# Optimization experiments

Measured on AMD Instinct MI355X. Metric: run time of the kernel, lower is better.

The kernel has to match this reference:

```python
import jax, jax.numpy as jnp
import numpy as np

B, T, E, H, V = 128, 64, 512, 1024, 10000


def setup_inputs() -> dict:
    key = jax.random.key(0)
    ks = jax.random.split(key, 9)
    s = 0.05
    return {
        "features": jax.random.normal(ks[0], (B, E), dtype=jnp.float32),
        "captions": jax.random.randint(ks[1], (B, T), 0, V, dtype=jnp.int64),
        "embed_W": jax.random.normal(ks[2], (V, E), dtype=jnp.float32) * s,
        "W_ih": jax.random.normal(ks[3], (4 * H, E), dtype=jnp.float32) * s,
        "W_hh": jax.random.normal(ks[4], (4 * H, H), dtype=jnp.float32) * s,
        "b_ih": jax.random.normal(ks[5], (4 * H,), dtype=jnp.float32) * s,
        "b_hh": jax.random.normal(ks[6], (4 * H,), dtype=jnp.float32) * s,
        "fc_W": jax.random.normal(ks[7], (V, H), dtype=jnp.float32) * s,
        "fc_b": jax.random.normal(ks[8], (V,), dtype=jnp.float32) * s,
    }


def reference(features, captions, embed_W, W_ih, W_hh, b_ih, b_hh, fc_W, fc_b):
    # Embed captions: [B, T, E]
    cap_emb = embed_W[captions]
    # Input sequence per the original loop: t=0 -> features, t>=1 -> cap_emb[:, t]
    xs = jnp.concatenate([features[:, None, :], cap_emb[:, 1:, :]], axis=1)  # [B, T, E]
    hdim = W_hh.shape[1]
    # Precompute input contribution to gates for all steps: [T, B, 4H]
    x_gates = jnp.einsum("bte,ge->tbg", xs, W_ih) + b_ih + b_hh

    def step(carry, xg):
        h, c = carry
        g = xg + h @ W_hh.T  # [B, 4H]
        i, f, gg, o = jnp.split(g, 4, axis=-1)
        i = jax.nn.sigmoid(i)
        f = jax.nn.sigmoid(f)
        gg = jnp.tanh(gg)
        o = jax.nn.sigmoid(o)
        c = f * c + i * gg
        h = o * jnp.tanh(c)
        return (h, c), h

    bsz = features.shape[0]
    h0 = jnp.zeros((bsz, hdim), dtype=features.dtype)
    c0 = jnp.zeros((bsz, hdim), dtype=features.dtype)
    _, hs = jax.lax.scan(step, (h0, c0), x_gates)  # hs: [T, B, H]
    # Output projection per step: [B, T, V]
    out = jnp.einsum("tbh,vh->btv", hs, fc_W) + fc_b
    return out
```

## Files before the change

### kernel.cpp

```cpp
#include <hip/hip_runtime.h>
#include <math.h>

static constexpr int Bb = 128;
static constexpr int Tt = 64;
static constexpr int Ee = 512;
static constexpr int Hh = 1024;
static constexpr int Vv = 10000;
static constexpr int G  = 4 * Hh;
static constexpr int Vpad = 10112;

typedef __attribute__((ext_vector_type(8))) short short8;
typedef __attribute__((ext_vector_type(4))) float floatx4;

__device__ __forceinline__ unsigned short f2bf(float f) {
    unsigned u = __float_as_uint(f);
    return (unsigned short)((u + 0x7fffu + ((u >> 16) & 1u)) >> 16);
}

__device__ __forceinline__ void gload16(const void* g, void* l) {
    __builtin_amdgcn_global_load_lds(
        (const __attribute__((address_space(1))) void*)g,
        (__attribute__((address_space(3))) void*)l, 16, 0, 0);
}

__device__ __forceinline__ float sigmoid_fast(float x) {
    return __builtin_amdgcn_rcpf(1.f + __expf(-x));
}
__device__ __forceinline__ float tanh_fast(float x) {
    float e = __expf(-2.f * fabsf(x));
    float t = (1.f - e) * __builtin_amdgcn_rcpf(1.f + e);
    return copysignf(t, x);
}

__global__ __launch_bounds__(256)
void cvt_bf16(const float* __restrict__ s, unsigned short* __restrict__ d,
              int n, int npad) {
    int i8 = (blockIdx.x * 256 + threadIdx.x) * 8;
    if (i8 >= npad) return;
    short8 v;
    #pragma unroll
    for (int j = 0; j < 8; ++j) {
        int e = i8 + j;
        float f = (e < n) ? s[e] : 0.f;
        v[j] = (short)f2bf(f);
    }
    *reinterpret_cast<short8*>(d + i8) = v;
}

__global__ __launch_bounds__(256)
void gather_xs(const float* __restrict__ features,
               const int* __restrict__ captions,
               const float* __restrict__ embed_W,
               unsigned short* __restrict__ xs) {
    int idx = blockIdx.x * 256 + threadIdx.x;
    int m  = idx >> 6;
    int c8 = (idx & 63) * 8;
    int t = m >> 7;
    int b = m & 127;
    const float* src;
    if (t == 0) {
        src = features + (size_t)b * Ee + c8;
    } else {
        int tok = captions[(size_t)b * Tt + t];
        src = embed_W + (size_t)tok * Ee + c8;
    }
    short8 v;
    #pragma unroll
    for (int j = 0; j < 8; ++j) v[j] = (short)f2bf(src[j]);
    *reinterpret_cast<short8*>(xs + (size_t)m * Ee + c8) = v;
}

template<int BM, int BN, int MODE>
__global__ __launch_bounds__(256)
void mfma_gemm(const unsigned short* __restrict__ A,
               const unsigned short* __restrict__ Bm,
               int M, int N, int K,
               const float* __restrict__ bias0, const float* __restrict__ bias1,
               float* __restrict__ C) {
    constexpr int BK = 32;
    constexpr int FM = BM / 32;
    constexpr int FN = BN / 32;
    __shared__ unsigned short As[BM * BK];
    __shared__ unsigned short Bs[BN * BK];

    const int nwg = gridDim.x * gridDim.y;
    const int flat = blockIdx.y * gridDim.x + blockIdx.x;
    const int tix = (flat & 7) * (nwg >> 3) + (flat >> 3);
    const int bx = tix % gridDim.x;
    const int by = tix / gridDim.x;

    const int tid  = threadIdx.x;
    const int wid  = tid >> 6;
    const int lane = tid & 63;
    const int wr = wid >> 1, wc = wid & 1;
    const int row0 = bx * BM;
    const int col0 = by * BN;
    const int l15 = lane & 15;
    const int kq  = lane >> 4;

    floatx4 acc[FM][FN];
    #pragma unroll
    for (int i = 0; i < FM; ++i)
        #pragma unroll
        for (int j = 0; j < FN; ++j) acc[i][j] = (floatx4)0.f;

    constexpr int LA = (BM * BK) / (256 * 8);
    constexpr int LB = (BN * BK) / (256 * 8);

    for (int k0 = 0; k0 < K; k0 += BK) {
        #pragma unroll
        for (int i = 0; i < LA; ++i) {
            int e = i * 2048 + tid * 8;
            int r = e >> 5, k = e & 31;
            gload16(A + (size_t)(row0 + r) * K + k0 + k, &As[e]);
        }
        #pragma unroll
        for (int i = 0; i < LB; ++i) {
            int e = i * 2048 + tid * 8;
            int r = e >> 5, k = e & 31;
            gload16(Bm + (size_t)(col0 + r) * K + k0 + k, &Bs[e]);
        }
        __syncthreads();

        short8 af[FM], bfr[FN];
        #pragma unroll
        for (int i = 0; i < FM; ++i) {
            int r = wr * (BM / 2) + i * 16 + l15;
            af[i] = *reinterpret_cast<const short8*>(&As[r * BK + kq * 8]);
        }
        #pragma unroll
        for (int j = 0; j < FN; ++j) {
            int c = wc * (BN / 2) + j * 16 + l15;
            bfr[j] = *reinterpret_cast<const short8*>(&Bs[c * BK + kq * 8]);
        }
        #pragma unroll
        for (int i = 0; i < FM; ++i)
            #pragma unroll
            for (int j = 0; j < FN; ++j)
                acc[i][j] = __builtin_amdgcn_mfma_f32_16x16x32_bf16(
                    af[i], bfr[j], acc[i][j], 0, 0, 0);
        __syncthreads();
    }

    #pragma unroll
    for (int i = 0; i < FM; ++i) {
        #pragma unroll
        for (int j = 0; j < FN; ++j) {
            #pragma unroll
            for (int q = 0; q < 4; ++q) {
                int m = row0 + wr * (BM / 2) + i * 16 + kq * 4 + q;
                int n = col0 + wc * (BN / 2) + j * 16 + l15;
                float v = acc[i][j][q];
                if (MODE == 0) {
                    C[(size_t)m * N + n] = v + bias0[n] + bias1[n];
                } else {
                    if (n < N) {
                        int t = m >> 7, b = m & 127;
                        C[(size_t)b * (Tt * Vv) + (size_t)t * Vv + n] = v + bias0[n];
                    }
                }
            }
        }
    }
}

__global__ __launch_bounds__(256)
void lstm_persist(const unsigned short* __restrict__ whhb,
                  const float* __restrict__ xg,
                  unsigned short* __restrict__ hsb,
                  unsigned* __restrict__ flags) {
    __shared__ unsigned short Wlds[64 * Hh];
    __shared__ float redsum[8 * 3 * 4 * 64];
    const int tid  = threadIdx.x;
    const int w    = blockIdx.x;
    const int wg_m = w & 3;
    const int wg_n = w >> 2;
    const int wave = tid >> 6;
    const int lane = tid & 63;
    const int l15  = lane & 15;
    const int kq   = lane >> 4;

    for (int i = 0; i < 32; ++i) {
        int e8 = i * 256 + tid;
        int q = e8 >> 6, gc = e8 & 63;
        int grow = (gc >> 4) * Hh + wg_n * 16 + (gc & 15);
        short8 v = *reinterpret_cast<const short8*>(
            whhb + (size_t)grow * Hh + q * 8);
        *reinterpret_cast<short8*>(&Wlds[(q * 64 + gc) * 8]) = v;
    }
    __syncthreads();

    const int row0 = wg_m * 32;
    const int hcol = wg_n * 16 + l15;
    const int lrA = (wave >> 1) * 16 + kq * 4 + ((wave & 1) * 2);
    const int lrB = lrA + 1;
    unsigned* myctr = flags + (size_t)(wg_m * 8 + (wg_n >> 3)) * 16;
    float cell0 = 0.f, cell1 = 0.f;

    float xa[2][4], xb[2][4];
    {
        const float* xrA = xg + (size_t)(row0 + lrA) * G + wg_n * 16 + l15;
        #pragma unroll
        for (int nb = 0; nb < 4; ++nb) {
            xa[0][nb] = xrA[nb * Hh];
            xa[1][nb] = xrA[G + nb * Hh];
        }
    }

#define WRC(W_, C_)                                                            \
    if (((C_) >> 1) != (W_)) {                                                 \
        _Pragma("unroll")                                                      \
        for (int nb = 0; nb < 4; ++nb)                                         \
            redsum[((C_) * 3 + (((W_) > ((C_) >> 1)) ? (W_)-1 : (W_))) * 256   \
                   + nb * 64 + lane] = acc[(C_) >> 2][nb][(C_) & 3];           \
    }

#define SPILL(W_)                                                              \
    do {                                                                       \
        _Pragma("unroll")                                                      \
        for (int nb = 0; nb < 4; ++nb) {                                       \
            own0[nb] = acc[(2 * (W_)) >> 2][nb][(2 * (W_)) & 3];               \
            own1[nb] = acc[(2 * (W_) + 1) >> 2][nb][(2 * (W_) + 1) & 3];       \
        }                                                                      \
        WRC(W_, 0); WRC(W_, 1); WRC(W_, 2); WRC(W_, 3);                        \
        WRC(W_, 4); WRC(W_, 5); WRC(W_, 6); WRC(W_, 7);                        \
    } while (0)

#define LSTM_STEP(T, XC, XN)                                                   \
    do {                                                                       \
        const int t_ = (T);                                                    \
        floatx4 acc[2][4];                                                     \
        _Pragma("unroll")                                                      \
        for (int i = 0; i < 2; ++i)                                            \
            _Pragma("unroll")                                                  \
            for (int j = 0; j < 4; ++j) acc[i][j] = (floatx4)0.f;              \
        if (t_ > 0) {                                                          \
            if (tid < 8) {                                                     \
                const unsigned* fl = flags + (size_t)(wg_m * 8 + tid) * 16;    \
                unsigned need = 8u * (unsigned)t_;                             \
                while (__hip_atomic_load(fl, __ATOMIC_RELAXED,                 \
                                         __HIP_MEMORY_SCOPE_AGENT) < need)     \
                    __builtin_amdgcn_s_sleep(1);                               \
            }                                                                  \
            __syncthreads();                                                   \
            asm volatile("" ::: "memory");                                     \
            const unsigned short* hprev = hsb + (size_t)(t_ - 1) * (Bb * Hh);  \
            const short8* ar0 = reinterpret_cast<const short8*>(               \
                hprev + (size_t)(row0 + l15) * Hh) + wave * 32 + kq;           \
            const short8* ar1 = reinterpret_cast<const short8*>(               \
                hprev + (size_t)(row0 + 16 + l15) * Hh) + wave * 32 + kq;      \
            short8 a0[8], a1[8];                                               \
            _Pragma("unroll")                                                  \
            for (int ks = 0; ks < 8; ++ks) a0[ks] = ar0[ks * 4];               \
            _Pragma("unroll")                                                  \
            for (int ks = 0; ks < 8; ++ks) a1[ks] = ar1[ks * 4];               \
            _Pragma("unroll")                                                  \
            for (int ks = 0; ks < 8; ++ks) {                                   \
                const short8* bp = reinterpret_cast<const short8*>(            \
                    &Wlds[((wave * 32 + ks * 4 + kq) * 64 + l15) * 8]);        \
                acc[0][0] = __builtin_amdgcn_mfma_f32_16x16x32_bf16(           \
                    a0[ks], bp[0], acc[0][0], 0, 0, 0);                        \
                acc[0][1] = __builtin_amdgcn_mfma_f32_16x16x32_bf16(           \
                    a0[ks], bp[16], acc[0][1], 0, 0, 0);                       \
                acc[0][2] = __builtin_amdgcn_mfma_f32_16x16x32_bf16(           \
                    a0[ks], bp[32], acc[0][2], 0, 0, 0);                       \
                acc[0][3] = __builtin_amdgcn_mfma_f32_16x16x32_bf16(           \
                    a0[ks], bp[48], acc[0][3], 0, 0, 0);                       \
            }                                                                  \
            _Pragma("unroll")                                                  \
            for (int ks = 0; ks < 8; ++ks) {                                   \
                const short8* bp = reinterpret_cast<const short8*>(            \
                    &Wlds[((wave * 32 + ks * 4 + kq) * 64 + l15) * 8]);        \
                acc[1][0] = __builtin_amdgcn_mfma_f32_16x16x32_bf16(           \
                    a1[ks], bp[0], acc[1][0], 0, 0, 0);                        \
                acc[1][1] = __builtin_amdgcn_mfma_f32_16x16x32_bf16(           \
                    a1[ks], bp[16], acc[1][1], 0, 0, 0);                       \
                acc[1][2] = __builtin_amdgcn_mfma_f32_16x16x32_bf16(           \
                    a1[ks], bp[32], acc[1][2], 0, 0, 0);                       \
                acc[1][3] = __builtin_amdgcn_mfma_f32_16x16x32_bf16(           \
                    a1[ks], bp[48], acc[1][3], 0, 0, 0);                       \
            }                                                                  \
        }                                                                      \
        float own0[4], own1[4];                                                \
        if (wave == 0)      SPILL(0);                                          \
        else if (wave == 1) SPILL(1);                                          \
        else if (wave == 2) SPILL(2);                                          \
        else                SPILL(3);                                          \
        __syncthreads();                                                       \
        float gA[4], gB[4];                                                    \
        {                                                                      \
            const int cA = wave * 2;                                           \
            _Pragma("unroll")                                                  \
            for (int nb = 0; nb < 4; ++nb) {                                   \
                int bA = (cA * 3) * 256 + nb * 64 + lane;                      \
                gA[nb] = own0[nb] + redsum[bA] + redsum[bA + 256]              \
                       + redsum[bA + 512] + XC[0][nb];                         \
                int bB = ((cA + 1) * 3) * 256 + nb * 64 + lane;                \
                gB[nb] = own1[nb] + redsum[bB] + redsum[bB + 256]              \
                       + redsum[bB + 512] + XC[1][nb];                         \
            }                                                                  \
        }                                                                      \
        unsigned short* ht = hsb + (size_t)t_ * (Bb * Hh);                     \
        {                                                                      \
            float si = sigmoid_fast(gA[0]);                                    \
            float sf = sigmoid_fast(gA[1]);                                    \
            float tg = tanh_fast(gA[2]);                                       \
            float so = sigmoid_fast(gA[3]);                                    \
            float cn = sf * cell0 + si * tg;                                   \
            cell0 = cn;                                                        \
            float h = so * tanh_fast(cn);                                      \
            __hip_atomic_store(&ht[(size_t)(row0 + lrA) * Hh + hcol], f2bf(h), \
                               __ATOMIC_RELAXED, __HIP_MEMORY_SCOPE_AGENT);    \
        }                                                                      \
        {                                                                      \
            float si = sigmoid_fast(gB[0]);                                    \
            float sf = sigmoid_fast(gB[1]);                                    \
            float tg = tanh_fast(gB[2]);                                       \
            float so = sigmoid_fast(gB[3]);                                    \
            float cn = sf * cell1 + si * tg;                                   \
            cell1 = cn;                                                        \
            float h = so * tanh_fast(cn);                                      \
            __hip_atomic_store(&ht[(size_t)(row0 + lrB) * Hh + hcol], f2bf(h), \
                               __ATOMIC_RELAXED, __HIP_MEMORY_SCOPE_AGENT);    \
        }                                                                      \
        __builtin_amdgcn_sched_barrier(0);                                     \
        if (t_ + 1 < Tt) {      \
            const float* xrA = xg + (size_t)(t_ + 1) * (Bb * G)                \
                + (size_t)(row0 + lrA) * G + wg_n * 16 + l15;                  \
            _Pragma("unroll")                                                  \
            for (int nb = 0; nb < 4; ++nb) {                                   \
                XN[0][nb] = xrA[nb * Hh];                                      \
                XN[1][nb] = xrA[G + nb * Hh];                                  \
            }                                                                  \
        }                                                                      \
        __builtin_amdgcn_sched_barrier(0);                                     \
        if (t_ < Tt - 1) {                                                     \
                \
            asm volatile("s_waitcnt vmcnt(8)" ::: "memory");                   \
            __builtin_amdgcn_sched_barrier(0);                                 \
            __builtin_amdgcn_s_barrier();                                      \
            __builtin_amdgcn_sched_barrier(0);                                 \
            if (tid == 0)                                                      \
                __hip_atomic_fetch_add(myctr, 1u, __ATOMIC_RELAXED,            \
                                       __HIP_MEMORY_SCOPE_AGENT);              \
        }                                                                      \
    } while (0)

    for (int tt = 0; tt < Tt; tt += 2) {
        LSTM_STEP(tt,     xa, xb);
        LSTM_STEP(tt + 1, xb, xa);
    }
#undef LSTM_STEP
#undef SPILL
#undef WRC
}

extern "C" void kernel_launch(void* const* d_in, const int* in_sizes, int n_in,
                              void* d_out, int out_size, void* d_ws, size_t ws_size,
                              hipStream_t stream) {
    const float* features = (const float*)d_in[0];
    const int*   captions = (const int*)d_in[1];
    const float* embed_W  = (const float*)d_in[2];
    const float* W_ih     = (const float*)d_in[3];
    const float* W_hh     = (const float*)d_in[4];
    const float* b_ih     = (const float*)d_in[5];
    const float* b_hh     = (const float*)d_in[6];
    const float* fc_W     = (const float*)d_in[7];
    const float* fc_b     = (const float*)d_in[8];
    float* out = (float*)d_out;

    unsigned short* xsb  = (unsigned short*)d_ws;
    unsigned short* wihb = xsb  + (size_t)Tt * Bb * Ee;
    unsigned short* whhb = wihb + (size_t)G * Ee;
    unsigned short* fcwb = whhb + (size_t)G * Hh;
    unsigned short* hsb  = fcwb + (size_t)Vpad * Hh;
    float* xg = (float*)(hsb + (size_t)Tt * Bb * Hh);
    unsigned* flags = (unsigned*)(xg + (size_t)Tt * Bb * G);

    hipMemsetAsync(flags, 0, 128 * 32 * sizeof(unsigned), stream);

    cvt_bf16<<<(G * Ee / 8) / 256, 256, 0, stream>>>(W_ih, wihb, G * Ee, G * Ee);
    cvt_bf16<<<(G * Hh / 8) / 256, 256, 0, stream>>>(W_hh, whhb, G * Hh, G * Hh);
    cvt_bf16<<<(Vpad * Hh / 8) / 256, 256, 0, stream>>>(fc_W, fcwb, Vv * Hh, Vpad * Hh);
    gather_xs<<<(Tt * Bb * (Ee / 8)) / 256, 256, 0, stream>>>(
        features, captions, embed_W, xsb);

    {
        dim3 grid(8192 / 128, G / 128);
        mfma_gemm<128, 128, 0><<<grid, 256, 0, stream>>>(
            xsb, wihb, 8192, G, Ee, b_ih, b_hh, xg);
    }

    lstm_persist<<<256, 256, 0, stream>>>(whhb, xg, hsb, flags);

    {
        dim3 grid(8192 / 128, Vpad / 128);
        mfma_gemm<128, 128, 2><<<grid, 256, 0, stream>>>(
            hsb, fcwb, 8192, Vv, Hh, fc_b, nullptr, out);
    }
}
```

Baseline: 751.1 us.

## Replace GEMM with 256x256 tile, 512-thread, 4-stage pipelined swizzled-LDS kernel

Replaces the 128x128 single-buffered MFMA GEMM with a 256x256 tile kernel using 8 waves and a 4-slot LDS ring. Global-to-LDS loads are prefetched two K-steps ahead, with split waits and barriers so loads overlap MFMA work. LDS reads use an XOR swizzle to avoid bank conflicts, and s_setprio raises priority around the MFMA blocks. Vpad grows to 10240 to fit the larger tile, which adds padded work and raises register and LDS pressure per block.

```diff
diff --git a/kernel.cpp b/kernel.cpp
--- a/kernel.cpp
+++ b/kernel.cpp
@@ -7,7 +7,7 @@
 static constexpr int Hh = 1024;
 static constexpr int Vv = 10000;
 static constexpr int G  = 4 * Hh;
-static constexpr int Vpad = 10112;
+static constexpr int Vpad = 10240;
 
 typedef __attribute__((ext_vector_type(8))) short short8;
 typedef __attribute__((ext_vector_type(4))) float floatx4;
@@ -70,18 +70,26 @@
     *reinterpret_cast<short8*>(xs + (size_t)m * Ee + c8) = v;
 }
 
-template<int BM, int BN, int MODE>
-__global__ __launch_bounds__(256)
-void mfma_gemm(const unsigned short* __restrict__ A,
-               const unsigned short* __restrict__ Bm,
-               int M, int N, int K,
-               const float* __restrict__ bias0, const float* __restrict__ bias1,
-               float* __restrict__ C) {
+__device__ __forceinline__ void stage_half(
+    const unsigned short* __restrict__ Gsrc, int Kdim, int rowbase, int k0,
+    unsigned short* ldsbase, int tid) {
+    int e = tid * 16;
+    int r = e >> 6;
+    int c = e & 63;
+    int c_log = c ^ ((r & 3) << 4);
+    gload16(Gsrc + (size_t)(rowbase + r) * Kdim + k0 + (c_log >> 1),
+            ldsbase + tid * 8);
+}
+
+template<int MODE>
+__global__ __launch_bounds__(512, 2)
+void gemm256(const unsigned short* __restrict__ A,
+             const unsigned short* __restrict__ Bm,
+             int M, int N, int K,
+             const float* __restrict__ bias0, const float* __restrict__ bias1,
+             float* __restrict__ C) {
     constexpr int BK = 32;
-    constexpr int FM = BM / 32;
-    constexpr int FN = BN / 32;
-    __shared__ unsigned short As[BM * BK];
-    __shared__ unsigned short Bs[BN * BK];
+    __shared__ unsigned short lds[4 * 2 * 256 * BK];
 
     const int nwg = gridDim.x * gridDim.y;
     const int flat = blockIdx.y * gridDim.x + blockIdx.x;
@@ -92,65 +100,94 @@
     const int tid  = threadIdx.x;
     const int wid  = tid >> 6;
     const int lane = tid & 63;
-    const int wr = wid >> 1, wc = wid & 1;
-    const int row0 = bx * BM;
-    const int col0 = by * BN;
+    const int wm = wid >> 2;
+    const int wn = wid & 3;
+    const int row0 = bx * 256;
+    const int col0 = by * 256;
     const int l15 = lane & 15;
     const int kq  = lane >> 4;
 
-    floatx4 acc[FM][FN];
+    const int NT = K / BK;
+
+    const int swz = (kq ^ (l15 & 3)) * 8;
+    const int arow_s = wm * 4096 + l15 * 32 + swz;
+    const int brow_s = 8192 + (wn >> 1) * 4096 + ((wn & 1) * 64 + l15) * 32 + swz;
+
+    floatx4 acc[8][4];
     #pragma unroll
-    for (int i = 0; i < FM; ++i)
-        #pragma unroll
-        for (int j = 0; j < FN; ++j) acc[i][j] = (floatx4)0.f;
-
-    constexpr int LA = (BM * BK) / (256 * 8);
-    constexpr int LB = (BN * BK) / (256 * 8);
-
-    for (int k0 = 0; k0 < K; k0 += BK) {
-        #pragma unroll
-        for (int i = 0; i < LA; ++i) {
-            int e = i * 2048 + tid * 8;
-            int r = e >> 5, k = e & 31;
-            gload16(A + (size_t)(row0 + r) * K + k0 + k, &As[e]);
+    for (int i = 0; i < 8; ++i)
+        #pragma unroll
+        for (int j = 0; j < 4; ++j) acc[i][j] = (floatx4)0.f;
+
+    stage_half(A,  K, row0,       0,  &lds[0],     tid);
+    stage_half(A,  K, row0 + 128, 0,  &lds[4096],  tid);
+    stage_half(Bm, K, col0,       0,  &lds[8192],  tid);
+    stage_half(Bm, K, col0 + 128, 0,  &lds[12288], tid);
+    stage_half(A,  K, row0,       BK, &lds[16384 + 0],     tid);
+    stage_half(A,  K, row0 + 128, BK, &lds[16384 + 4096],  tid);
+    stage_half(Bm, K, col0,       BK, &lds[16384 + 8192],  tid);
+    stage_half(Bm, K, col0 + 128, BK, &lds[16384 + 12288], tid);
+    asm volatile("s_waitcnt vmcnt(4)" ::: "memory");
+    asm volatile("s_barrier" ::: "memory");
+
+    for (int t = 0; t < NT; ++t) {
+        const int cur = (t & 3) * 16384;
+        short8 af[4], bfr[4];
+        #pragma unroll
+        for (int fi = 0; fi < 4; ++fi)
+            af[fi] = *reinterpret_cast<const short8*>(&lds[cur + arow_s + fi * 512]);
+        #pragma unroll
+        for (int fj = 0; fj < 4; ++fj)
+            bfr[fj] = *reinterpret_cast<const short8*>(&lds[cur + brow_s + fj * 512]);
+        if (t + 2 < NT) {
+            const int nb = ((t + 2) & 3) * 16384;
+            stage_half(A, K, row0,       (t + 2) * BK, &lds[nb],        tid);
+            stage_half(A, K, row0 + 128, (t + 2) * BK, &lds[nb + 4096], tid);
         }
-        #pragma unroll
-        for (int i = 0; i < LB; ++i) {
-            int e = i * 2048 + tid * 8;
-            int r = e >> 5, k = e & 31;
-            gload16(Bm + (size_t)(col0 + r) * K + k0 + k, &Bs[e]);
+        asm volatile("s_barrier" ::: "memory");
+        __builtin_amdgcn_s_setprio(1);
+        #pragma unroll
+        for (int fi = 0; fi < 4; ++fi)
+            #pragma unroll
+            for (int fj = 0; fj < 4; ++fj)
+                acc[fi][fj] = __builtin_amdgcn_mfma_f32_16x16x32_bf16(
+                    af[fi], bfr[fj], acc[fi][fj], 0, 0, 0);
+        __builtin_amdgcn_s_setprio(0);
+        asm volatile("s_barrier" ::: "memory");
+        #pragma unroll
+        for (int fi = 0; fi < 4; ++fi)
+            af[fi] = *reinterpret_cast<const short8*>(
+                &lds[cur + arow_s + (fi + 4) * 512]);
+        if (t + 2 < NT) {
+            const int nb = ((t + 2) & 3) * 16384 + 8192;
+            stage_half(Bm, K, col0,       (t + 2) * BK, &lds[nb],        tid);
+            stage_half(Bm, K, col0 + 128, (t + 2) * BK, &lds[nb + 4096], tid);
         }
-        __syncthreads();
-
-        short8 af[FM], bfr[FN];
-        #pragma unroll
-        for (int i = 0; i < FM; ++i) {
-            int r = wr * (BM / 2) + i * 16 + l15;
-            af[i] = *reinterpret_cast<const short8*>(&As[r * BK + kq * 8]);
+        asm volatile("s_barrier" ::: "memory");
+        __builtin_amdgcn_s_setprio(1);
+        #pragma unroll
+        for (int fi = 0; fi < 4; ++fi)
+            #pragma unroll
+            for (int fj = 0; fj < 4; ++fj)
+                acc[fi + 4][fj] = __builtin_amdgcn_mfma_f32_16x16x32_bf16(
+                    af[fi], bfr[fj], acc[fi + 4][fj], 0, 0, 0);
+        __builtin_amdgcn_s_setprio(0);
+        if (t + 1 < NT) {
+            if (t + 2 < NT) asm volatile("s_waitcnt vmcnt(4)" ::: "memory");
+            else            asm volatile("s_waitcnt vmcnt(0)" ::: "memory");
         }
-        #pragma unroll
-        for (int j = 0; j < FN; ++j) {
-            int c = wc * (BN / 2) + j * 16 + l15;
-            bfr[j] = *reinterpret_cast<const short8*>(&Bs[c * BK + kq * 8]);
-        }
-        #pragma unroll
-        for (int i = 0; i < FM; ++i)
-            #pragma unroll
-            for (int j = 0; j < FN; ++j)
-                acc[i][j] = __builtin_amdgcn_mfma_f32_16x16x32_bf16(
-                    af[i], bfr[j], acc[i][j], 0, 0, 0);
-        __syncthreads();
+        asm volatile("s_barrier" ::: "memory");
     }
 
     #pragma unroll
-    for (int i = 0; i < FM; ++i) {
-        #pragma unroll
-        for (int j = 0; j < FN; ++j) {
+    for (int fi = 0; fi < 8; ++fi) {
+        #pragma unroll
+        for (int fj = 0; fj < 4; ++fj) {
             #pragma unroll
             for (int q = 0; q < 4; ++q) {
-                int m = row0 + wr * (BM / 2) + i * 16 + kq * 4 + q;
-                int n = col0 + wc * (BN / 2) + j * 16 + l15;
-                float v = acc[i][j][q];
+                int m = row0 + wm * 128 + fi * 16 + kq * 4 + q;
+                int n = col0 + wn * 64 + fj * 16 + l15;
+                float v = acc[fi][fj][q];
                 if (MODE == 0) {
                     C[(size_t)m * N + n] = v + bias0[n] + bias1[n];
                 } else {
@@ -377,7 +414,7 @@
     float* xg = (float*)(hsb + (size_t)Tt * Bb * Hh);
     unsigned* flags = (unsigned*)(xg + (size_t)Tt * Bb * G);
 
-    hipMemsetAsync(flags, 0, 128 * 32 * sizeof(unsigned), stream);
+    (void)hipMemsetAsync(flags, 0, 128 * 32 * sizeof(unsigned), stream);
 
     cvt_bf16<<<(G * Ee / 8) / 256, 256, 0, stream>>>(W_ih, wihb, G * Ee, G * Ee);
     cvt_bf16<<<(G * Hh / 8) / 256, 256, 0, stream>>>(W_hh, whhb, G * Hh, G * Hh);
@@ -386,16 +423,16 @@
         features, captions, embed_W, xsb);
 
     {
-        dim3 grid(8192 / 128, G / 128);
-        mfma_gemm<128, 128, 0><<<grid, 256, 0, stream>>>(
+        dim3 grid(8192 / 256, G / 256);
+        gemm256<0><<<grid, 512, 0, stream>>>(
             xsb, wihb, 8192, G, Ee, b_ih, b_hh, xg);
     }
 
     lstm_persist<<<256, 256, 0, stream>>>(whhb, xg, hsb, flags);
 
     {
-        dim3 grid(8192 / 128, Vpad / 128);
-        mfma_gemm<128, 128, 2><<<grid, 256, 0, stream>>>(
+        dim3 grid(8192 / 256, Vpad / 256);
+        gemm256<2><<<grid, 512, 0, stream>>>(
             hsb, fcwb, 8192, Vv, Hh, fc_b, nullptr, out);
     }
 }
```

Result: faster. 692.2 us (-7.8%).
